# Kernel tuning notes

Hardware: AMD Instinct MI355X
Metric: run time of the kernel (lower is better)

The kernel has to match this reference:

```python
import jax, jax.numpy as jnp
import numpy as np
from jax import lax

WS = 32          # region_size
N = WS * WS      # tokens per region = 1024
H = 8            # num_heads
HD = 64          # head_dim
C = H * HD       # dim = 512
B = 8            # num_regions * batch
K = 15           # conv_k
SCALE = HD ** -0.5


def _rel_index():
    # Swin relative position index, computed statically with numpy.
    coords = np.stack(np.meshgrid(np.arange(WS), np.arange(WS), indexing='ij'))  # [2,WS,WS]
    flat = coords.reshape(2, -1)                                                 # [2,N]
    rel = (flat[:, :, None] - flat[:, None, :]).transpose(1, 2, 0)               # [N,N,2]
    rel = rel.copy()
    rel[..., 0] += WS - 1
    rel[..., 1] += WS - 1
    rel[..., 0] *= 2 * WS - 1
    return rel.sum(-1)  # [N,N] int

_REL_IDX = jnp.asarray(_rel_index())


def setup_inputs() -> dict:
    key = jax.random.key(0)
    ks = jax.random.split(key, 6)
    return {
        'x': jax.random.normal(ks[0], (B, N, C), dtype=jnp.float32),
        'w_qkv': jax.random.normal(ks[1], (3 * C, C), dtype=jnp.float32) * 0.02,
        'b_qkv': jnp.zeros((3 * C,), dtype=jnp.float32),
        'w_proj': jax.random.normal(ks[2], (C, C), dtype=jnp.float32) * 0.02,
        'b_proj': jnp.zeros((C,), dtype=jnp.float32),
        'rel_table': jax.random.normal(ks[3], ((2 * WS - 1) ** 2, H), dtype=jnp.float32) * 0.02,
        'pe_w': jax.random.normal(ks[4], (H, 1, K, 1), dtype=jnp.float32) * 0.02,
        'pe_b': jnp.zeros((H,), dtype=jnp.float32),
    }


def reference(x, w_qkv, b_qkv, w_proj, b_proj, rel_table, pe_w, pe_b):
    b, n, c = x.shape
    qkv = (x @ w_qkv.T + b_qkv).reshape(b, n, 3, H, HD)
    q = jnp.moveaxis(qkv[:, :, 0], 2, 1)  # [B,H,N,HD]
    k = jnp.moveaxis(qkv[:, :, 1], 2, 1)
    v = jnp.moveaxis(qkv[:, :, 2], 2, 1)

    attn = jnp.einsum('bhnd,bhmd->bhnm', q * SCALE, k)  # [B,H,N,N]

    # depthwise (per-head) conv over the query axis of the attention matrix, kernel (K,1)
    pe = lax.conv_general_dilated(
        attn, pe_w, window_strides=(1, 1), padding=[(K // 2, K // 2), (0, 0)],
        dimension_numbers=('NCHW', 'OIHW', 'NCHW'), feature_group_count=H,
    ) + pe_b[None, :, None, None]
    attn = attn + pe

    # relative position bias gather: [N*N] -> [N,N,H] -> [H,N,N]
    bias = rel_table[_REL_IDX.reshape(-1)].reshape(n, n, H).transpose(2, 0, 1)
    attn = jax.nn.softmax(attn + bias[None], axis=-1)

    out = jnp.einsum('bhnm,bhmd->bnhd', attn, v).reshape(b, n, c)
    return out @ w_proj.T + b_proj
```

## Files before the change

### kernel.cpp

```cpp
#include <hip/hip_runtime.h>

typedef __bf16 bf16x8 __attribute__((ext_vector_type(8)));
typedef float f32x4 __attribute__((ext_vector_type(4)));
typedef unsigned short u16;
typedef unsigned int u32;
typedef unsigned long long u64;

__device__ __forceinline__ float bf2f(u16 x){ u32 u = ((u32)x)<<16; return __builtin_bit_cast(float,u); }
__device__ __forceinline__ u16 f2bf(float f){ u32 u = __builtin_bit_cast(u32,f); u = (u + 0x7fffu + ((u>>16)&1u)) >> 16; return (u16)u; }

__device__ __forceinline__ void glds16(const u16* g, u16* l){
  __builtin_amdgcn_global_load_lds((const __attribute__((address_space(1))) u32*)g,
                                   (__attribute__((address_space(3))) u32*)l, 16, 0, 0);
}

static constexpr float L2E = 1.4426950408889634f;
static constexpr float QSC = 0.125f * 1.4426950408889634f;

__global__ void k_cvtall(const float* __restrict__ x, const float* __restrict__ wq,
                         const float* __restrict__ wp, const float* __restrict__ rt,
                         u16* __restrict__ xo, u16* __restrict__ wqo,
                         u16* __restrict__ wpo, u64* __restrict__ rel2){
  int bid = blockIdx.x;
  if (bid < 5120){
    int i = bid*256 + threadIdx.x;
    const float* s; u16* d; int base;
    if (i < 1048576){ s=x; d=xo; base=0; }
    else if (i < 1245184){ s=wq; d=wqo; base=1048576; }
    else { s=wp; d=wpo; base=1245184; }
    int j = i - base;
    float4 v = reinterpret_cast<const float4*>(s)[j];
    reinterpret_cast<ushort4*>(d)[j] = make_ushort4(f2bf(v.x),f2bf(v.y),f2bf(v.z),f2bf(v.w));
  } else {
    int i = (bid-5120)*256 + threadIdx.x;
    if (i < 31752){
      int h = i / 3969, i2 = i - h*3969;
      u64 v = 0;
      #pragma unroll
      for (int j=0;j<4;j++){
        int idx = i2-3+j;
        u16 bb = 0;
        if (idx >= 0) bb = f2bf(rt[idx*8+h]*L2E);
        v |= (u64)bb << (16*j);
      }
      rel2[i] = v;
    }
  }
}

__device__ __forceinline__ void acc8(float* acc, uint4 v, float w){
  acc[0]=fmaf(w, bf2f((u16)(v.x)),     acc[0]); acc[1]=fmaf(w, bf2f((u16)(v.x>>16)), acc[1]);
  acc[2]=fmaf(w, bf2f((u16)(v.y)),     acc[2]); acc[3]=fmaf(w, bf2f((u16)(v.y>>16)), acc[3]);
  acc[4]=fmaf(w, bf2f((u16)(v.z)),     acc[4]); acc[5]=fmaf(w, bf2f((u16)(v.z>>16)), acc[5]);
  acc[6]=fmaf(w, bf2f((u16)(v.w)),     acc[6]); acc[7]=fmaf(w, bf2f((u16)(v.w>>16)), acc[7]);
}

template<int MODE>
__global__ __launch_bounds__(256) void k_gemm(
  const u16* __restrict__ A, const u16* __restrict__ Bw, const float* __restrict__ bias,
  u16* __restrict__ qo, u16* __restrict__ ko, u16* __restrict__ vo, float* __restrict__ co)
{
  constexpr int K = 512;
  constexpr int BM = (MODE==0) ? 128 : 64;
  constexpr int NX = (MODE==0) ? 12 : 4;
  constexpr int CPX = NX*(8192/BM)/8;
  constexpr int NF = (MODE==0) ? 4 : 2;
  __shared__ __align__(16) u16 lA[3][BM*32];
  __shared__ __align__(16) u16 lB[3][4096];
  const int lin = blockIdx.y*NX + blockIdx.x;
  const int swz = (lin&7)*CPX + (lin>>3);
  const int i0 = (swz/NX)*BM, j0 = (swz%NX)*128;
  const int T = threadIdx.x;
  const int w = T>>6, lane = T&63, g = lane>>4, cl = lane&15;
  const int wr = (MODE==0) ? (w>>1)*64 : 0;
  const int wc = (MODE==0) ? (w&1)*64 : w*32;
  const int sr = T>>2, sk = 8*(T&3);
  f32x4 acc[4][NF];
  #pragma unroll
  for (int a=0;a<4;a++)
    #pragma unroll
    for (int b=0;b<NF;b++) acc[a][b] = (f32x4){0.f,0.f,0.f,0.f};

  auto STAGE = [&](int t, u16* bA, u16* bB){
    glds16(A  + (long)(i0+sr)*K    + t*32 + sk, bA + 8*T);
    if (MODE==0) glds16(A + (long)(i0+64+sr)*K + t*32 + sk, bA + 2048 + 8*T);
    glds16(Bw + (long)(j0+sr)*K    + t*32 + sk, bB + 8*T);
    glds16(Bw + (long)(j0+64+sr)*K + t*32 + sk, bB + 2048 + 8*T);
  };
  STAGE(0, lA[0], lB[0]);
  STAGE(1, lA[1], lB[1]);
  int cur = 0, sb = 2;
  for (int t=0;t<16;t++){
    if (t<15){
      if (MODE==0) asm volatile("s_waitcnt vmcnt(4)" ::: "memory");
      else         asm volatile("s_waitcnt vmcnt(3)" ::: "memory");
    } else {
      asm volatile("s_waitcnt vmcnt(0)" ::: "memory");
    }
    __builtin_amdgcn_s_barrier();
    asm volatile("" ::: "memory");
    if (t<14) STAGE(t+2, lA[sb], lB[sb]);
    const u16* cA = lA[cur];
    const u16* cB = lB[cur];
    bf16x8 af[4], bfr[NF];
    #pragma unroll
    for (int mf=0;mf<4;mf++) af[mf]  = *reinterpret_cast<const bf16x8*>(cA + (wr+16*mf+cl)*32 + 8*g);
    #pragma unroll
    for (int nf=0;nf<NF;nf++) bfr[nf] = *reinterpret_cast<const bf16x8*>(cB + (wc+16*nf+cl)*32 + 8*g);
    __builtin_amdgcn_s_setprio(1);
    #pragma unroll
    for (int mf=0;mf<4;mf++)
      #pragma unroll
      for (int nf=0;nf<NF;nf++)
        acc[mf][nf] = __builtin_amdgcn_mfma_f32_16x16x32_bf16(af[mf], bfr[nf], acc[mf][nf], 0,0,0);
    __builtin_amdgcn_s_setprio(0);
    cur = (cur==2)?0:cur+1;
    sb  = (sb==2)?0:sb+1;
  }

  #pragma unroll
  for (int mf=0;mf<4;mf++){
    #pragma unroll
    for (int nf=0;nf<NF;nf++){
      const int col = j0 + wc + 16*nf + cl;
      const float bb = bias[col];
      const int row0 = i0 + wr + 16*mf + 4*g;
      if (MODE==0){
        const int part = col>>9, h=(col>>6)&7, dd=col&63;
        const int b = row0>>10, n0 = row0&1023, bh = b*8+h;
        if (part==2){
          const int a32 = n0 & ~31, G = (n0>>2)&7;
          const int stb = ((G&3)<<3) | ((G>>2)<<2);
          ushort4 pk = make_ushort4(f2bf(acc[mf][nf][0]+bb), f2bf(acc[mf][nf][1]+bb),
                                    f2bf(acc[mf][nf][2]+bb), f2bf(acc[mf][nf][3]+bb));
          *reinterpret_cast<ushort4*>(vo + ((long)bh*64+dd)*1024 + a32 + stb) = pk;
        } else {
          #pragma unroll
          for (int e=0;e<4;e++){
            float v = acc[mf][nf][e] + bb;
            if (part==0) qo[((long)bh*1024+n0+e)*64+dd] = f2bf(v*QSC);
            else         ko[((long)bh*1024+n0+e)*64+dd] = f2bf(v);
          }
        }
      } else {
        #pragma unroll
        for (int e=0;e<4;e++)
          co[(long)(row0+e)*512 + col] = acc[mf][nf][e] + bb;
      }
    }
  }
}

__global__ __launch_bounds__(256,2) void k_attn(
  const u16* __restrict__ Qp, const u16* __restrict__ Kb, const u16* __restrict__ VT,
  const u64* __restrict__ relT2, const float* __restrict__ pw, u16* __restrict__ Ao)
{
  __shared__ __align__(16) u16 kls[4][4096];
  __shared__ __align__(16) u16 vls[4][4096];
  const int bid = blockIdx.x;
  const int xcd = bid&7, slot = bid>>3;
  const int bh = xcd*8 + (slot>>3), rb = slot&7;
  const int b = bh>>3, h = bh&7;
  const int T = threadIdx.x, w=T>>6, lane=T&63, g=lane>>4, cl=lane&15;
  const int rowbase = rb*128 + w*32;
  const int qr0 = rowbase + cl, qr1 = rowbase + 16 + cl;
  const u16* Qbh = Qp + (long)bh*65536;
  const u16* Kbh = Kb + (long)bh*65536;
  const u16* Vbh = VT + (long)bh*65536;

  bf16x8 qf[2][2];
  {
    const int rowstart = rb*128 - 8;
    u16* qs = &kls[0][0];
    #pragma unroll
    for (int s=0;s<5;s++){
      int idx = s*256 + T;
      if (idx < 1152){
        int row = idx>>3, u = idx&7;
        int gr = rowstart + row; gr = gr < 0 ? 0 : (gr > 1023 ? 1023 : gr);
        glds16(Qbh + gr*64 + ((u ^ (row&7))<<3), qs + idx*8);
      }
    }
    asm volatile("s_waitcnt vmcnt(0)" ::: "memory");
    __builtin_amdgcn_s_barrier();
    asm volatile("" ::: "memory");
    float wgt[15];
    #pragma unroll
    for (int t=0;t<15;t++) wgt[t] = pw[h*15+t];
    #pragma unroll
    for (int G=0;G<2;G++){
      const int r = rowbase + 16*G + cl;
      const int lr = r - rowstart;
      #pragma unroll
      for (int s2=0;s2<2;s2++){
        const int ub = 4*s2 + g;
        float a[8];
        {
          uint4 cv = *reinterpret_cast<const uint4*>(qs + lr*64 + ((ub ^ (lr&7))<<3));
          a[0]=bf2f((u16)cv.x); a[1]=bf2f((u16)(cv.x>>16));
          a[2]=bf2f((u16)cv.y); a[3]=bf2f((u16)(cv.y>>16));
          a[4]=bf2f((u16)cv.z); a[5]=bf2f((u16)(cv.z>>16));
          a[6]=bf2f((u16)cv.w); a[7]=bf2f((u16)(cv.w>>16));
        }
        #pragma unroll
        for (int t=0;t<15;t++){
          int nn = r - 7 + t;
          if (nn >= 0 && nn < 1024){
            int lrow = lr - 7 + t;
            uint4 v = *reinterpret_cast<const uint4*>(qs + lrow*64 + ((ub ^ (lrow&7))<<3));
            acc8(a, v, wgt[t]);
          }
        }
        bf16x8 qq;
        #pragma unroll
        for (int j=0;j<8;j++) qq[j] = (__bf16)a[j];
        qf[G][s2] = qq;
      }
    }
    __builtin_amdgcn_s_barrier();
    asm volatile("" ::: "memory");
  }

  const int rt[2] = { (qr0>>5)*63 + (qr0&31) + 1984,
                      (qr1>>5)*63 + (qr1&31) + 1984 };
  const u64* relTh = relT2 + h*3969;
  float lsum[2] = {0.f, 0.f};
  f32x4 oacc[2][4];
  #pragma unroll
  for (int G=0;G<2;G++)
    #pragma unroll
    for (int c=0;c<4;c++) oacc[G][c] = (f32x4){0.f,0.f,0.f,0.f};

  auto STAGE = [&](int m0, int bi){
    #pragma unroll
    for (int s=0;s<2;s++){
      int idx = s*256 + T, row = idx>>3, u = idx&7, sw = (u ^ (row&7))<<3;
      glds16(Kbh + (m0+row)*64 + sw,         kls[bi] + idx*8);
      glds16(Vbh + (long)row*1024 + m0 + sw, vls[bi] + idx*8);
    }
  };
  auto QK = [&](const char* kb, f32x4 (&sacc)[2][4]){
    #pragma unroll
    for (int G=0;G<2;G++)
      #pragma unroll
      for (int c=0;c<4;c++) sacc[G][c] = (f32x4){0.f,0.f,0.f,0.f};
    #pragma unroll
    for (int c=0;c<4;c++){
      const int r = 16*c + cl, rs = r&7;
      const char* kr = kb + r*128;
      bf16x8 kf0 = *reinterpret_cast<const bf16x8*>(kr + ((g    ^rs)<<4));
      bf16x8 kf1 = *reinterpret_cast<const bf16x8*>(kr + (((4+g)^rs)<<4));
      #pragma unroll
      for (int G=0;G<2;G++){
        sacc[G][c] = __builtin_amdgcn_mfma_f32_16x16x32_bf16(kf0, qf[G][0], sacc[G][c],0,0,0);
        sacc[G][c] = __builtin_amdgcn_mfma_f32_16x16x32_bf16(kf1, qf[G][1], sacc[G][c],0,0,0);
      }
    }
  };
  auto RELLOAD = [&](int t, u64 (&rx)[2][4]){
    #pragma unroll
    for (int G=0;G<2;G++)
      #pragma unroll
      for (int c=0;c<4;c++){
        const int kk = (t<<6) + 16*c + 4*g;
        rx[G][c] = relTh[rt[G] - ((kk>>5)*63 + (kk&31))];
      }
  };
  auto SMPV = [&](const char* vb, f32x4 (&sacc)[2][4], u64 (&rx)[2][4]){
    float p[2][4][4];
    #pragma unroll
    for (int G=0;G<2;G++)
      #pragma unroll
      for (int c=0;c<4;c++){
        const u32 lo = (u32)rx[G][c], hi = (u32)(rx[G][c]>>32);
        const float b0 = __builtin_bit_cast(float, hi & 0xffff0000u);
        const float b1 = __builtin_bit_cast(float, hi << 16);
        const float b2 = __builtin_bit_cast(float, lo & 0xffff0000u);
        const float b3 = __builtin_bit_cast(float, lo << 16);
        p[G][c][0] = __builtin_amdgcn_exp2f(sacc[G][c][0] + b0);
        p[G][c][1] = __builtin_amdgcn_exp2f(sacc[G][c][1] + b1);
        p[G][c][2] = __builtin_amdgcn_exp2f(sacc[G][c][2] + b2);
        p[G][c][3] = __builtin_amdgcn_exp2f(sacc[G][c][3] + b3);
      }
    #pragma unroll
    for (int G=0;G<2;G++)
      #pragma unroll
      for (int c=0;c<4;c++) lsum[G] += (p[G][c][0]+p[G][c][1]) + (p[G][c][2]+p[G][c][3]);
    bf16x8 pa[2][2];
    #pragma unroll
    for (int G=0;G<2;G++)
      #pragma unroll
      for (int e=0;e<4;e++){
        pa[G][0][e]   = (__bf16)p[G][0][e];  pa[G][0][4+e] = (__bf16)p[G][1][e];
        pa[G][1][e]   = (__bf16)p[G][2][e];  pa[G][1][4+e] = (__bf16)p[G][3][e];
      }
    #pragma unroll
    for (int ks=0;ks<2;ks++)
      #pragma unroll
      for (int c2=0;c2<4;c2++){
        const int dd = 16*c2 + cl, dsw = dd&7;
        bf16x8 vf = *reinterpret_cast<const bf16x8*>(vb + dd*128 + (((4*ks+g)^dsw)<<4));
        #pragma unroll
        for (int G=0;G<2;G++)
          oacc[G][c2] = __builtin_amdgcn_mfma_f32_16x16x32_bf16(pa[G][ks], vf, oacc[G][c2],0,0,0);
      }
  };

  f32x4 saccA[2][4], saccB[2][4];
  u64 rxA[2][4], rxB[2][4];

  STAGE(0,0); STAGE(64,1);
  asm volatile("s_waitcnt vmcnt(0)" ::: "memory");
  __builtin_amdgcn_s_barrier();
  asm volatile("" ::: "memory");

  for (int p=0;p<8;p++){
    const int t0 = 2*p, t1 = t0+1;
    if (p<7){ STAGE((t0+2)<<6, (t0+2)&3); STAGE((t1+2)<<6, (t1+2)&3); }
    asm volatile("" ::: "memory");
    RELLOAD(t0, rxA);
    RELLOAD(t1, rxB);
    __builtin_amdgcn_s_setprio(1);
    QK((const char*)kls[t0&3], saccA);
    QK((const char*)kls[t1&3], saccB);
    SMPV((const char*)vls[t0&3], saccA, rxA);
    SMPV((const char*)vls[t1&3], saccB, rxB);
    __builtin_amdgcn_s_setprio(0);
    if (p<7){
      asm volatile("s_waitcnt vmcnt(0)" ::: "memory");
      __builtin_amdgcn_s_barrier();
      asm volatile("" ::: "memory");
    }
  }

  #pragma unroll
  for (int G=0;G<2;G++){
    lsum[G] += __shfl_xor(lsum[G], 16, 64);
    lsum[G] += __shfl_xor(lsum[G], 32, 64);
  }
  #pragma unroll
  for (int G=0;G<2;G++)
    #pragma unroll
    for (int e=0;e<4;e++){
      float inv = 1.0f/__shfl(lsum[G], 4*g+e, 64);
      const long orow = (long)b*1024 + rowbase + 16*G + 4*g + e;
      #pragma unroll
      for (int c2=0;c2<4;c2++)
        Ao[orow*512 + h*64 + 16*c2 + cl] = f2bf(oacc[G][c2][e]*inv);
    }
}

extern "C" void kernel_launch(void* const* d_in, const int* in_sizes, int n_in,
                              void* d_out, int out_size, void* d_ws, size_t ws_size,
                              hipStream_t stream)
{
  const float* x         = (const float*)d_in[0];
  const float* w_qkv     = (const float*)d_in[1];
  const float* b_qkv     = (const float*)d_in[2];
  const float* w_proj    = (const float*)d_in[3];
  const float* b_proj    = (const float*)d_in[4];
  const float* rel_table = (const float*)d_in[5];
  const float* pe_w      = (const float*)d_in[6];
  (void)in_sizes; (void)n_in; (void)out_size; (void)ws_size;

  u16* ws    = (u16*)d_ws;
  u16* x_bf  = ws;
  u16* wq_bf = x_bf  + 4194304;
  u16* wp_bf = wq_bf + 786432;
  u16* q_bf  = wp_bf + 262144;
  u16* k_bf  = q_bf  + 4194304;
  u16* vt_bf = k_bf  + 4194304;
  u16* ao_bf = vt_bf + 4194304;
  u64* relT2 = (u64*)(ao_bf + 4194304);

  k_cvtall<<<5245,256,0,stream>>>(x, w_qkv, w_proj, rel_table, x_bf, wq_bf, wp_bf, relT2);
  k_gemm<0><<<dim3(12,64),256,0,stream>>>(x_bf, wq_bf, b_qkv, q_bf, k_bf, vt_bf, nullptr);
  k_attn<<<512,256,0,stream>>>(q_bf, k_bf, vt_bf, relT2, pe_w, ao_bf);
  k_gemm<1><<<dim3(4,128),256,0,stream>>>(ao_bf, wp_bf, b_proj, nullptr, nullptr, nullptr, (float*)d_out);
}
```

Baseline: 78.30 us.

## Use 8 waves of 16 query rows per attention block instead of 4×32

The attention kernel now launches 512 threads per block, and each wave owns 16 query rows instead of 32. Each block still covers 128 rows and stages the same K/V tiles, so the staging work per thread is halved and per-thread register state (accumulators, relative-bias values, Q fragments) shrinks by half. The goal is more resident waves per CU to hide LDS and global latency. In exchange, each K/V fragment read from LDS feeds only one MFMA row group rather than two, which doubles LDS read traffic per unit of compute.

```diff
diff --git a/kernel.cpp b/kernel.cpp
--- a/kernel.cpp
+++ b/kernel.cpp
@@ -151,7 +151,7 @@
   }
 }
 
-__global__ __launch_bounds__(256,2) void k_attn(
+__global__ __launch_bounds__(512,4) void k_attn(
   const u16* __restrict__ Qp, const u16* __restrict__ Kb, const u16* __restrict__ VT,
   const u64* __restrict__ relT2, const float* __restrict__ pw, u16* __restrict__ Ao)
 {
@@ -162,19 +162,19 @@
   const int bh = xcd*8 + (slot>>3), rb = slot&7;
   const int b = bh>>3, h = bh&7;
   const int T = threadIdx.x, w=T>>6, lane=T&63, g=lane>>4, cl=lane&15;
-  const int rowbase = rb*128 + w*32;
-  const int qr0 = rowbase + cl, qr1 = rowbase + 16 + cl;
+  const int rowbase = rb*128 + w*16;
+  const int qr = rowbase + cl;
   const u16* Qbh = Qp + (long)bh*65536;
   const u16* Kbh = Kb + (long)bh*65536;
   const u16* Vbh = VT + (long)bh*65536;
 
-  bf16x8 qf[2][2];
+  bf16x8 qf[2];
   {
     const int rowstart = rb*128 - 8;
     u16* qs = &kls[0][0];
     #pragma unroll
-    for (int s=0;s<5;s++){
-      int idx = s*256 + T;
+    for (int s=0;s<3;s++){
+      int idx = s*512 + T;
       if (idx < 1152){
         int row = idx>>3, u = idx&7;
         int gr = rowstart + row; gr = gr < 0 ? 0 : (gr > 1023 ? 1023 : gr);
@@ -187,127 +187,104 @@
     float wgt[15];
     #pragma unroll
     for (int t=0;t<15;t++) wgt[t] = pw[h*15+t];
-    #pragma unroll
-    for (int G=0;G<2;G++){
-      const int r = rowbase + 16*G + cl;
-      const int lr = r - rowstart;
-      #pragma unroll
-      for (int s2=0;s2<2;s2++){
-        const int ub = 4*s2 + g;
-        float a[8];
-        {
-          uint4 cv = *reinterpret_cast<const uint4*>(qs + lr*64 + ((ub ^ (lr&7))<<3));
-          a[0]=bf2f((u16)cv.x); a[1]=bf2f((u16)(cv.x>>16));
-          a[2]=bf2f((u16)cv.y); a[3]=bf2f((u16)(cv.y>>16));
-          a[4]=bf2f((u16)cv.z); a[5]=bf2f((u16)(cv.z>>16));
-          a[6]=bf2f((u16)cv.w); a[7]=bf2f((u16)(cv.w>>16));
+    const int lr = qr - rowstart;
+    #pragma unroll
+    for (int s2=0;s2<2;s2++){
+      const int ub = 4*s2 + g;
+      float a[8];
+      {
+        uint4 cv = *reinterpret_cast<const uint4*>(qs + lr*64 + ((ub ^ (lr&7))<<3));
+        a[0]=bf2f((u16)cv.x); a[1]=bf2f((u16)(cv.x>>16));
+        a[2]=bf2f((u16)cv.y); a[3]=bf2f((u16)(cv.y>>16));
+        a[4]=bf2f((u16)cv.z); a[5]=bf2f((u16)(cv.z>>16));
+        a[6]=bf2f((u16)cv.w); a[7]=bf2f((u16)(cv.w>>16));
+      }
+      #pragma unroll
+      for (int t=0;t<15;t++){
+        int nn = qr - 7 + t;
+        if (nn >= 0 && nn < 1024){
+          int lrow = lr - 7 + t;
+          uint4 v = *reinterpret_cast<const uint4*>(qs + lrow*64 + ((lrow&7)<<3 ^ (ub<<3)));
+          acc8(a, v, wgt[t]);
         }
-        #pragma unroll
-        for (int t=0;t<15;t++){
-          int nn = r - 7 + t;
-          if (nn >= 0 && nn < 1024){
-            int lrow = lr - 7 + t;
-            uint4 v = *reinterpret_cast<const uint4*>(qs + lrow*64 + ((ub ^ (lrow&7))<<3));
-            acc8(a, v, wgt[t]);
-          }
-        }
-        bf16x8 qq;
-        #pragma unroll
-        for (int j=0;j<8;j++) qq[j] = (__bf16)a[j];
-        qf[G][s2] = qq;
-      }
+      }
+      bf16x8 qq;
+      #pragma unroll
+      for (int j=0;j<8;j++) qq[j] = (__bf16)a[j];
+      qf[s2] = qq;
     }
     __builtin_amdgcn_s_barrier();
     asm volatile("" ::: "memory");
   }
 
-  const int rt[2] = { (qr0>>5)*63 + (qr0&31) + 1984,
-                      (qr1>>5)*63 + (qr1&31) + 1984 };
+  const int rt = (qr>>5)*63 + (qr&31) + 1984;
   const u64* relTh = relT2 + h*3969;
-  float lsum[2] = {0.f, 0.f};
-  f32x4 oacc[2][4];
+  float lsum = 0.f;
+  f32x4 oacc[4];
   #pragma unroll
-  for (int G=0;G<2;G++)
-    #pragma unroll
-    for (int c=0;c<4;c++) oacc[G][c] = (f32x4){0.f,0.f,0.f,0.f};
+  for (int c=0;c<4;c++) oacc[c] = (f32x4){0.f,0.f,0.f,0.f};
 
   auto STAGE = [&](int m0, int bi){
-    #pragma unroll
-    for (int s=0;s<2;s++){
-      int idx = s*256 + T, row = idx>>3, u = idx&7, sw = (u ^ (row&7))<<3;
-      glds16(Kbh + (m0+row)*64 + sw,         kls[bi] + idx*8);
-      glds16(Vbh + (long)row*1024 + m0 + sw, vls[bi] + idx*8);
-    }
-  };
-  auto QK = [&](const char* kb, f32x4 (&sacc)[2][4]){
-    #pragma unroll
-    for (int G=0;G<2;G++)
-      #pragma unroll
-      for (int c=0;c<4;c++) sacc[G][c] = (f32x4){0.f,0.f,0.f,0.f};
+    int row = T>>3, u = T&7, sw = (u ^ (row&7))<<3;
+    glds16(Kbh + (m0+row)*64 + sw,         kls[bi] + T*8);
+    glds16(Vbh + (long)row*1024 + m0 + sw, vls[bi] + T*8);
+  };
+  auto QK = [&](const char* kb, f32x4 (&sacc)[4]){
+    #pragma unroll
+    for (int c=0;c<4;c++) sacc[c] = (f32x4){0.f,0.f,0.f,0.f};
     #pragma unroll
     for (int c=0;c<4;c++){
       const int r = 16*c + cl, rs = r&7;
       const char* kr = kb + r*128;
       bf16x8 kf0 = *reinterpret_cast<const bf16x8*>(kr + ((g    ^rs)<<4));
       bf16x8 kf1 = *reinterpret_cast<const bf16x8*>(kr + (((4+g)^rs)<<4));
-      #pragma unroll
-      for (int G=0;G<2;G++){
-        sacc[G][c] = __builtin_amdgcn_mfma_f32_16x16x32_bf16(kf0, qf[G][0], sacc[G][c],0,0,0);
-        sacc[G][c] = __builtin_amdgcn_mfma_f32_16x16x32_bf16(kf1, qf[G][1], sacc[G][c],0,0,0);
-      }
-    }
-  };
-  auto RELLOAD = [&](int t, u64 (&rx)[2][4]){
-    #pragma unroll
-    for (int G=0;G<2;G++)
-      #pragma unroll
-      for (int c=0;c<4;c++){
-        const int kk = (t<<6) + 16*c + 4*g;
-        rx[G][c] = relTh[rt[G] - ((kk>>5)*63 + (kk&31))];
-      }
-  };
-  auto SMPV = [&](const char* vb, f32x4 (&sacc)[2][4], u64 (&rx)[2][4]){
-    float p[2][4][4];
-    #pragma unroll
-    for (int G=0;G<2;G++)
-      #pragma unroll
-      for (int c=0;c<4;c++){
-        const u32 lo = (u32)rx[G][c], hi = (u32)(rx[G][c]>>32);
-        const float b0 = __builtin_bit_cast(float, hi & 0xffff0000u);
-        const float b1 = __builtin_bit_cast(float, hi << 16);
-        const float b2 = __builtin_bit_cast(float, lo & 0xffff0000u);
-        const float b3 = __builtin_bit_cast(float, lo << 16);
-        p[G][c][0] = __builtin_amdgcn_exp2f(sacc[G][c][0] + b0);
-        p[G][c][1] = __builtin_amdgcn_exp2f(sacc[G][c][1] + b1);
-        p[G][c][2] = __builtin_amdgcn_exp2f(sacc[G][c][2] + b2);
-        p[G][c][3] = __builtin_amdgcn_exp2f(sacc[G][c][3] + b3);
-      }
-    #pragma unroll
-    for (int G=0;G<2;G++)
-      #pragma unroll
-      for (int c=0;c<4;c++) lsum[G] += (p[G][c][0]+p[G][c][1]) + (p[G][c][2]+p[G][c][3]);
-    bf16x8 pa[2][2];
-    #pragma unroll
-    for (int G=0;G<2;G++)
-      #pragma unroll
-      for (int e=0;e<4;e++){
-        pa[G][0][e]   = (__bf16)p[G][0][e];  pa[G][0][4+e] = (__bf16)p[G][1][e];
-        pa[G][1][e]   = (__bf16)p[G][2][e];  pa[G][1][4+e] = (__bf16)p[G][3][e];
-      }
-    #pragma unroll
-    for (int ks=0;ks<2;ks++)
+      sacc[c] = __builtin_amdgcn_mfma_f32_16x16x32_bf16(kf0, qf[0], sacc[c],0,0,0);
+      sacc[c] = __builtin_amdgcn_mfma_f32_16x16x32_bf16(kf1, qf[1], sacc[c],0,0,0);
+    }
+  };
+  auto RELLOAD = [&](int t, u64 (&rx)[4]){
+    #pragma unroll
+    for (int c=0;c<4;c++){
+      const int kk = (t<<6) + 16*c + 4*g;
+      rx[c] = relTh[rt - ((kk>>5)*63 + (kk&31))];
+    }
+  };
+  auto SMPV = [&](const char* vb, f32x4 (&sacc)[4], u64 (&rx)[4]){
+    float p[4][4];
+    #pragma unroll
+    for (int c=0;c<4;c++){
+      const u32 lo = (u32)rx[c], hi = (u32)(rx[c]>>32);
+      const float b0 = __builtin_bit_cast(float, hi & 0xffff0000u);
+      const float b1 = __builtin_bit_cast(float, hi << 16);
+      const float b2 = __builtin_bit_cast(float, lo & 0xffff0000u);
+      const float b3 = __builtin_bit_cast(float, lo << 16);
+      p[c][0] = __builtin_amdgcn_exp2f(sacc[c][0] + b0);
+      p[c][1] = __builtin_amdgcn_exp2f(sacc[c][1] + b1);
+      p[c][2] = __builtin_amdgcn_exp2f(sacc[c][2] + b2);
+      p[c][3] = __builtin_amdgcn_exp2f(sacc[c][3] + b3);
+    }
+    #pragma unroll
+    for (int c=0;c<4;c++) lsum += (p[c][0]+p[c][1]) + (p[c][2]+p[c][3]);
+    bf16x8 pa0, pa1;
+    #pragma unroll
+    for (int e=0;e<4;e++){
+      pa0[e]   = (__bf16)p[0][e];  pa0[4+e] = (__bf16)p[1][e];
+      pa1[e]   = (__bf16)p[2][e];  pa1[4+e] = (__bf16)p[3][e];
+    }
+    #pragma unroll
+    for (int ks=0;ks<2;ks++){
+      const bf16x8 pa = ks ? pa1 : pa0;
       #pragma unroll
       for (int c2=0;c2<4;c2++){
         const int dd = 16*c2 + cl, dsw = dd&7;
         bf16x8 vf = *reinterpret_cast<const bf16x8*>(vb + dd*128 + (((4*ks+g)^dsw)<<4));
-        #pragma unroll
-        for (int G=0;G<2;G++)
-          oacc[G][c2] = __builtin_amdgcn_mfma_f32_16x16x32_bf16(pa[G][ks], vf, oacc[G][c2],0,0,0);
-      }
-  };
-
-  f32x4 saccA[2][4], saccB[2][4];
-  u64 rxA[2][4], rxB[2][4];
+        oacc[c2] = __builtin_amdgcn_mfma_f32_16x16x32_bf16(pa, vf, oacc[c2],0,0,0);
+      }
+    }
+  };
+
+  f32x4 saccA[4], saccB[4];
+  u64 rxA[4], rxB[4];
 
   STAGE(0,0); STAGE(64,1);
   asm volatile("s_waitcnt vmcnt(0)" ::: "memory");
@@ -333,21 +310,16 @@
     }
   }
 
+  lsum += __shfl_xor(lsum, 16, 64);
+  lsum += __shfl_xor(lsum, 32, 64);
   #pragma unroll
-  for (int G=0;G<2;G++){
-    lsum[G] += __shfl_xor(lsum[G], 16, 64);
-    lsum[G] += __shfl_xor(lsum[G], 32, 64);
-  }
-  #pragma unroll
-  for (int G=0;G<2;G++)
-    #pragma unroll
-    for (int e=0;e<4;e++){
-      float inv = 1.0f/__shfl(lsum[G], 4*g+e, 64);
-      const long orow = (long)b*1024 + rowbase + 16*G + 4*g + e;
-      #pragma unroll
-      for (int c2=0;c2<4;c2++)
-        Ao[orow*512 + h*64 + 16*c2 + cl] = f2bf(oacc[G][c2][e]*inv);
-    }
+  for (int e=0;e<4;e++){
+    float inv = 1.0f/__shfl(lsum, 4*g+e, 64);
+    const long orow = (long)b*1024 + rowbase + 4*g + e;
+    #pragma unroll
+    for (int c2=0;c2<4;c2++)
+      Ao[orow*512 + h*64 + 16*c2 + cl] = f2bf(oacc[c2][e]*inv);
+  }
 }
 
 extern "C" void kernel_launch(void* const* d_in, const int* in_sizes, int n_in,
@@ -375,6 +347,6 @@
 
   k_cvtall<<<5245,256,0,stream>>>(x, w_qkv, w_proj, rel_table, x_bf, wq_bf, wp_bf, relT2);
   k_gemm<0><<<dim3(12,64),256,0,stream>>>(x_bf, wq_bf, b_qkv, q_bf, k_bf, vt_bf, nullptr);
-  k_attn<<<512,256,0,stream>>>(q_bf, k_bf, vt_bf, relT2, pe_w, ao_bf);
+  k_attn<<<512,512,0,stream>>>(q_bf, k_bf, vt_bf, relT2, pe_w, ao_bf);
   k_gemm<1><<<dim3(4,128),256,0,stream>>>(ao_bf, wp_bf, b_proj, nullptr, nullptr, nullptr, (float*)d_out);
 }
```

After: 76.84 us (median of 2 runs). About the same (-1.9%).

## Halve LDS ring to double buffer and raise attention occupancy to four blocks

Applied to the files above, without the earlier changes.

The attention kernel drops its four-deep K/V LDS ring, which processed two 64-key tiles per iteration, in favour of a two-deep ring processing one tile per iteration. Shared memory falls from 64KB to 32KB per block and launch bounds go from 2 to 4 blocks per CU, so more waves can hide latency. In exchange each tile now needs its own barrier, there is less unrolled work to interleave between barriers, and the compiler must fit the higher occupancy into a smaller register budget.

```diff
diff --git a/kernel.cpp b/kernel.cpp
--- a/kernel.cpp
+++ b/kernel.cpp
@@ -151,12 +151,11 @@
   }
 }
 
-__global__ __launch_bounds__(256,2) void k_attn(
+__global__ __launch_bounds__(256,4) void k_attn(
   const u16* __restrict__ Qp, const u16* __restrict__ Kb, const u16* __restrict__ VT,
   const u64* __restrict__ relT2, const float* __restrict__ pw, u16* __restrict__ Ao)
 {
-  __shared__ __align__(16) u16 kls[4][4096];
-  __shared__ __align__(16) u16 vls[4][4096];
+  __shared__ __align__(16) u16 smem[16384];
   const int bid = blockIdx.x;
   const int xcd = bid&7, slot = bid>>3;
   const int bh = xcd*8 + (slot>>3), rb = slot&7;
@@ -171,7 +170,7 @@
   bf16x8 qf[2][2];
   {
     const int rowstart = rb*128 - 8;
-    u16* qs = &kls[0][0];
+    u16* qs = smem;
     #pragma unroll
     for (int s=0;s<5;s++){
       int idx = s*256 + T;
@@ -235,15 +234,35 @@
     #pragma unroll
     for (int s=0;s<2;s++){
       int idx = s*256 + T, row = idx>>3, u = idx&7, sw = (u ^ (row&7))<<3;
-      glds16(Kbh + (m0+row)*64 + sw,         kls[bi] + idx*8);
-      glds16(Vbh + (long)row*1024 + m0 + sw, vls[bi] + idx*8);
+      glds16(Kbh + (m0+row)*64 + sw,         smem + bi*4096 + idx*8);
+      glds16(Vbh + (long)row*1024 + m0 + sw, smem + 8192 + bi*4096 + idx*8);
     }
   };
-  auto QK = [&](const char* kb, f32x4 (&sacc)[2][4]){
+
+  STAGE(0,0);
+
+  for (int t=0;t<16;t++){
+    u64 rx[2][4];
+    #pragma unroll
+    for (int G=0;G<2;G++)
+      #pragma unroll
+      for (int c=0;c<4;c++){
+        const int kk = (t<<6) + 16*c + 4*g;
+        rx[G][c] = relTh[rt[G] - ((kk>>5)*63 + (kk&31))];
+      }
+    asm volatile("s_waitcnt vmcnt(8)" ::: "memory");
+    __builtin_amdgcn_s_barrier();
+    asm volatile("" ::: "memory");
+    if (t<15) STAGE((t+1)<<6, (t+1)&1);
+
+    const char* kb = (const char*)(smem + (t&1)*4096);
+    const char* vb = (const char*)(smem + 8192 + (t&1)*4096);
+    f32x4 sacc[2][4];
     #pragma unroll
     for (int G=0;G<2;G++)
       #pragma unroll
       for (int c=0;c<4;c++) sacc[G][c] = (f32x4){0.f,0.f,0.f,0.f};
+    __builtin_amdgcn_s_setprio(1);
     #pragma unroll
     for (int c=0;c<4;c++){
       const int r = 16*c + cl, rs = r&7;
@@ -256,17 +275,6 @@
         sacc[G][c] = __builtin_amdgcn_mfma_f32_16x16x32_bf16(kf1, qf[G][1], sacc[G][c],0,0,0);
       }
     }
-  };
-  auto RELLOAD = [&](int t, u64 (&rx)[2][4]){
-    #pragma unroll
-    for (int G=0;G<2;G++)
-      #pragma unroll
-      for (int c=0;c<4;c++){
-        const int kk = (t<<6) + 16*c + 4*g;
-        rx[G][c] = relTh[rt[G] - ((kk>>5)*63 + (kk&31))];
-      }
-  };
-  auto SMPV = [&](const char* vb, f32x4 (&sacc)[2][4], u64 (&rx)[2][4]){
     float p[2][4][4];
     #pragma unroll
     for (int G=0;G<2;G++)
@@ -304,33 +312,7 @@
         for (int G=0;G<2;G++)
           oacc[G][c2] = __builtin_amdgcn_mfma_f32_16x16x32_bf16(pa[G][ks], vf, oacc[G][c2],0,0,0);
       }
-  };
-
-  f32x4 saccA[2][4], saccB[2][4];
-  u64 rxA[2][4], rxB[2][4];
-
-  STAGE(0,0); STAGE(64,1);
-  asm volatile("s_waitcnt vmcnt(0)" ::: "memory");
-  __builtin_amdgcn_s_barrier();
-  asm volatile("" ::: "memory");
-
-  for (int p=0;p<8;p++){
-    const int t0 = 2*p, t1 = t0+1;
-    if (p<7){ STAGE((t0+2)<<6, (t0+2)&3); STAGE((t1+2)<<6, (t1+2)&3); }
-    asm volatile("" ::: "memory");
-    RELLOAD(t0, rxA);
-    RELLOAD(t1, rxB);
-    __builtin_amdgcn_s_setprio(1);
-    QK((const char*)kls[t0&3], saccA);
-    QK((const char*)kls[t1&3], saccB);
-    SMPV((const char*)vls[t0&3], saccA, rxA);
-    SMPV((const char*)vls[t1&3], saccB, rxB);
     __builtin_amdgcn_s_setprio(0);
-    if (p<7){
-      asm volatile("s_waitcnt vmcnt(0)" ::: "memory");
-      __builtin_amdgcn_s_barrier();
-      asm volatile("" ::: "memory");
-    }
   }
 
   #pragma unroll
```

Result: no change. 78.57 us (+0.3%).
